# Optimization experiments

Hardware: AMD Instinct MI355X
Metric: run time of the kernel (lower is better)

Reference implementation:

```python
import jax, jax.numpy as jnp
import numpy as np

N, E, IN, HID, OUT = 50000, 800000, 128, 128, 4
EPS = 1e-16  # PyG softmax denominator epsilon


def setup_inputs() -> dict:
    key = jax.random.key(0)
    ks = jax.random.split(key, 12)
    g = lambda k, shp, fan: jax.random.normal(k, shp, jnp.float32) * (1.0 / np.sqrt(fan))
    return {
        "x": jax.random.normal(ks[0], (N, IN), jnp.float32),
        "edge_index": jax.random.randint(ks[1], (2, E), 0, N),
        "W1": g(ks[2], (IN, HID), IN),
        "att_l1": g(ks[3], (HID,), HID),
        "att_r1": g(ks[4], (HID,), HID),
        "b1": jnp.zeros((HID,), jnp.float32),
        "W2": g(ks[5], (HID, HID), HID),
        "att_l2": g(ks[6], (HID,), HID),
        "att_r2": g(ks[7], (HID,), HID),
        "b2": jnp.zeros((HID,), jnp.float32),
        "Wc": g(ks[8], (2 * HID, OUT), 2 * HID),
        "bc": jnp.zeros((OUT,), jnp.float32),
    }


def supergat_layer(x, src, dst, W, att_l, att_r, b, n_nodes):
    """SuperGATConv, attention_type='MX', heads=1, concat, eval mode (no dropout)."""
    h = x @ W                                   # [N, C] linear transform (no bias)
    hj, hi = h[src], h[dst]                     # gather source / target feats per edge [E', C]
    logits = jnp.sum(hi * hj, axis=-1)          # MX dot-product logits [E']
    alpha = hj @ att_l + hi @ att_r             # GAT-style additive score [E']
    alpha = alpha * jax.nn.sigmoid(logits)      # MX gating
    # segment softmax over destination node
    amax = jax.ops.segment_max(alpha, dst, num_segments=n_nodes)
    ea = jnp.exp(alpha - amax[dst])
    denom = jax.ops.segment_sum(ea, dst, num_segments=n_nodes)
    w = ea / (denom[dst] + EPS)
    # scatter-aggregate weighted messages
    out = jax.ops.segment_sum(hj * w[:, None], dst, num_segments=n_nodes)
    return out + b


def reference(x, edge_index, W1, att_l1, att_r1, b1, W2, att_l2, att_r2, b2, Wc, bc):
    row, col = edge_index[0], edge_index[1]
    loop = jnp.arange(N)
    src = jnp.concatenate([row, loop])          # add self-loops (PyG default)
    dst = jnp.concatenate([col, loop])
    h = supergat_layer(x, src, dst, W1, att_l1, att_r1, b1, N)
    h = jax.nn.relu(h)
    h = supergat_layer(h, src, dst, W2, att_l2, att_r2, b2, N)
    edge_emb = jnp.concatenate([h[row], h[col]], axis=-1)  # [E, 2*HID]
    return edge_emb @ Wc + bc                    # [E, OUT]
```

## Files before the change

### kernel.cpp

```cpp
#include <hip/hip_runtime.h>
#include <hip/hip_fp16.h>
#include <math.h>

#define C 128
#define EPSV 1e-16f
#define BCAP 64

typedef _Float16 half2v __attribute__((ext_vector_type(2)));
typedef _Float16 half8v __attribute__((ext_vector_type(8)));
typedef float float4v __attribute__((ext_vector_type(4)));

__device__ __forceinline__ float fdot2(half2v a, half2v b, float c) {
#if __has_builtin(__builtin_amdgcn_fdot2)
    return __builtin_amdgcn_fdot2(a, b, c, false);
#else
    return c + (float)a.x * (float)b.x + (float)a.y * (float)b.y;
#endif
}

__device__ __forceinline__ void unpack8(uint4 a, uint4 b, half2v* h) {
    h[0] = __builtin_bit_cast(half2v, a.x);
    h[1] = __builtin_bit_cast(half2v, a.y);
    h[2] = __builtin_bit_cast(half2v, a.z);
    h[3] = __builtin_bit_cast(half2v, a.w);
    h[4] = __builtin_bit_cast(half2v, b.x);
    h[5] = __builtin_bit_cast(half2v, b.y);
    h[6] = __builtin_bit_cast(half2v, b.z);
    h[7] = __builtin_bit_cast(half2v, b.w);
}


__global__ __launch_bounds__(256) void zero_kernel(int* __restrict__ p, int n) {
    int i = blockIdx.x * 256 + threadIdx.x;
    if (i < n) p[i] = 0;
}

__global__ __launch_bounds__(256) void fill_kernel(const int* __restrict__ rowA, const int* __restrict__ colA,
                                                   int* __restrict__ cursor, int* __restrict__ bucket, int e) {
    int i = blockIdx.x * 256 + threadIdx.x;
    if (i < e) {
        int c = colA[i];
        int p = atomicAdd(&cursor[c], 1);
        if (p < BCAP) bucket[c * BCAP + p] = rowA[i];
    }
}


template <bool SRC16>
__global__ __launch_bounds__(256) void gemm_att_mfma(const void* __restrict__ Asrc, const float* __restrict__ W,
                                                     const float* __restrict__ attl, const float* __restrict__ attr,
                                                     __half* __restrict__ Hh, float* __restrict__ al,
                                                     float* __restrict__ ar, int M) {
    __shared__ __half Ah[64][136];
    __shared__ __half Wt[128][136];

    int t = threadIdx.x;
    int lane = t & 63;
    int w = t >> 6;
    int quad = lane >> 4;
    int n16 = lane & 15;
    int row0 = blockIdx.x * 64;

    {
        int k = t >> 1;
        int cbase = (t & 1) * 64;
        const float4* Wr = (const float4*)(W + (size_t)k * C + cbase);
        #pragma unroll
        for (int q = 0; q < 16; q++) {
            float4 wv = Wr[q];
            int c = cbase + q * 4;
            Wt[c][k]     = __float2half(wv.x);
            Wt[c + 1][k] = __float2half(wv.y);
            Wt[c + 2][k] = __float2half(wv.z);
            Wt[c + 3][k] = __float2half(wv.w);
        }
    }
    {
        int r = t >> 2;
        int ks = (t & 3) * 32;
        int gr = row0 + r;
        if (SRC16) {
            const uint4* src = (const uint4*)((const __half*)Asrc + (size_t)gr * C + ks);
            uint4 z = make_uint4(0, 0, 0, 0);
            #pragma unroll
            for (int q = 0; q < 4; q++) {
                uint4 v = (gr < M) ? src[q] : z;
                *(uint4*)&Ah[r][ks + q * 8] = v;
            }
        } else {
            const float4* src = (const float4*)((const float*)Asrc + (size_t)gr * C + ks);
            #pragma unroll
            for (int q = 0; q < 8; q++) {
                float4 v = (gr < M) ? src[q] : make_float4(0.f, 0.f, 0.f, 0.f);
                __half2 lo = __floats2half2_rn(v.x, v.y);
                __half2 hi2 = __floats2half2_rn(v.z, v.w);
                uint2 pk;
                pk.x = *(unsigned int*)&lo;
                pk.y = *(unsigned int*)&hi2;
                *(uint2*)&Ah[r][ks + q * 4] = pk;
            }
        }
    }
    __syncthreads();

    float4v acc[8];
    #pragma unroll
    for (int ct = 0; ct < 8; ct++) acc[ct] = (float4v){0.f, 0.f, 0.f, 0.f};
    int mrow = w * 16 + n16;
    #pragma unroll
    for (int ks = 0; ks < 4; ks++) {
        int k0 = ks * 32 + quad * 8;
        half8v a = *(half8v*)&Ah[mrow][k0];
        #pragma unroll
        for (int ct = 0; ct < 8; ct++) {
            half8v b = *(half8v*)&Wt[ct * 16 + n16][k0];
            acc[ct] = __builtin_amdgcn_mfma_f32_16x16x32_f16(a, b, acc[ct], 0, 0, 0);
        }
    }

    #pragma unroll
    for (int ct = 0; ct < 8; ct++) {
        #pragma unroll
        for (int r = 0; r < 4; r++) {
            Ah[w * 16 + quad * 4 + r][ct * 16 + n16] = __float2half(acc[ct][r]);
        }
    }
    __syncthreads();

    {
        int r = t >> 2;
        int seg = (t & 3) * 32;
        int gr = row0 + r;
        uint4 d[4];
        #pragma unroll
        for (int q = 0; q < 4; q++) d[q] = *(uint4*)&Ah[r][seg + q * 8];
        float pl = 0.f, pr = 0.f;
        #pragma unroll
        for (int q = 0; q < 4; q++) {
            half2v hv[4];
            hv[0] = __builtin_bit_cast(half2v, d[q].x);
            hv[1] = __builtin_bit_cast(half2v, d[q].y);
            hv[2] = __builtin_bit_cast(half2v, d[q].z);
            hv[3] = __builtin_bit_cast(half2v, d[q].w);
            #pragma unroll
            for (int j = 0; j < 4; j++) {
                float2 f = make_float2((float)hv[j].x, (float)hv[j].y);
                int c = seg + q * 8 + j * 2;
                pl += f.x * attl[c] + f.y * attl[c + 1];
                pr += f.x * attr[c] + f.y * attr[c + 1];
            }
        }
        if (gr < M) {
            uint4* dst = (uint4*)&Hh[(size_t)gr * C + seg];
            #pragma unroll
            for (int q = 0; q < 4; q++) dst[q] = d[q];
        }
        pl += __shfl_xor(pl, 1);
        pl += __shfl_xor(pl, 2);
        pr += __shfl_xor(pr, 1);
        pr += __shfl_xor(pr, 2);
        if ((t & 3) == 0 && gr < M) { al[gr] = pl; ar[gr] = pr; }
    }
}


__device__ __forceinline__ void agg_core8(const __half* __restrict__ Hh, const int* __restrict__ bucket,
                                          const int* __restrict__ cnt, const float* __restrict__ al,
                                          const float* __restrict__ ar, const float* __restrict__ bvec,
                                          int node, int sub, int k, float* out) {
    const uint4* hp = (const uint4*)&Hh[(size_t)node * C + 16 * k];
    uint4 ha = hp[0], hb = hp[1];
    half2v hi[8];
    unpack8(ha, hb, hi);

    float aln = al[node];
    float arn = ar[node];

    float ds = 0.f;
    #pragma unroll
    for (int j = 0; j < 8; j++) ds = fdot2(hi[j], hi[j], ds);
    ds += __shfl_xor(ds, 1);
    ds += __shfl_xor(ds, 2);
    ds += __shfl_xor(ds, 4);
    float pself = __expf((aln + arn) / (1.0f + __expf(-ds)));

    bool s0 = (sub == 0);
    float denom = s0 ? pself : 0.0f;
    float acc[16];
    #pragma unroll
    for (int j = 0; j < 8; j++) {
        acc[2 * j]     = s0 ? pself * (float)hi[j].x : 0.0f;
        acc[2 * j + 1] = s0 ? pself * (float)hi[j].y : 0.0f;
    }

    int deg = cnt[node];
    if (deg > BCAP) deg = BCAP;
    int base = node * BCAP;

    int i = sub;
    uint4 raC, rbC;
    float alsC = 0.f;
    if (i < deg) {
        int s = bucket[base + i];
        const uint4* rp = (const uint4*)&Hh[(size_t)s * C + 16 * k];
        raC = rp[0];
        rbC = rp[1];
        alsC = al[s];
    }
    while (i < deg) {
        uint4 ra = raC, rb = rbC;
        float als = alsC;
        int inext = i + 8;
        if (inext < deg) {
            int s = bucket[base + inext];
            const uint4* rp = (const uint4*)&Hh[(size_t)s * C + 16 * k];
            raC = rp[0];
            rbC = rp[1];
            alsC = al[s];
        }
        half2v hj[8];
        unpack8(ra, rb, hj);
        float d = 0.f;
        #pragma unroll
        for (int j = 0; j < 8; j++) d = fdot2(hi[j], hj[j], d);
        d += __shfl_xor(d, 1);
        d += __shfl_xor(d, 2);
        d += __shfl_xor(d, 4);
        float p = __expf((als + arn) / (1.0f + __expf(-d)));
        denom += p;
        #pragma unroll
        for (int j = 0; j < 8; j++) {
            acc[2 * j]     += p * (float)hj[j].x;
            acc[2 * j + 1] += p * (float)hj[j].y;
        }
        i = inext;
    }

    denom += __shfl_xor(denom, 8);
    denom += __shfl_xor(denom, 16);
    denom += __shfl_xor(denom, 32);
    #pragma unroll
    for (int off = 8; off <= 32; off <<= 1) {
        #pragma unroll
        for (int j = 0; j < 16; j++) acc[j] += __shfl_xor(acc[j], off);
    }

    float inv = 1.0f / (denom + EPSV);
    const float4* bp = (const float4*)&bvec[16 * k];
    float4 b0 = bp[0], b1 = bp[1], b2 = bp[2], b3 = bp[3];
    out[0] = acc[0] * inv + b0.x;   out[1] = acc[1] * inv + b0.y;
    out[2] = acc[2] * inv + b0.z;   out[3] = acc[3] * inv + b0.w;
    out[4] = acc[4] * inv + b1.x;   out[5] = acc[5] * inv + b1.y;
    out[6] = acc[6] * inv + b1.z;   out[7] = acc[7] * inv + b1.w;
    out[8] = acc[8] * inv + b2.x;   out[9] = acc[9] * inv + b2.y;
    out[10] = acc[10] * inv + b2.z; out[11] = acc[11] * inv + b2.w;
    out[12] = acc[12] * inv + b3.x; out[13] = acc[13] * inv + b3.y;
    out[14] = acc[14] * inv + b3.z; out[15] = acc[15] * inv + b3.w;
}

__global__ __launch_bounds__(256) void agg_kernel(const __half* __restrict__ Hh, const int* __restrict__ bucket,
                                                  const int* __restrict__ cnt, const float* __restrict__ al,
                                                  const float* __restrict__ ar, const float* __restrict__ bvec,
                                                  __half* __restrict__ O, int n) {
    int node = blockIdx.x * 4 + (threadIdx.x >> 6);
    int lane = threadIdx.x & 63;
    if (node >= n) return;
    int sub = lane >> 3;
    int k = lane & 7;
    float out[16];
    agg_core8(Hh, bucket, cnt, al, ar, bvec, node, sub, k, out);
    if (sub == 0) {
        uint4 pk[2];
        #pragma unroll
        for (int h = 0; h < 2; h++) {
            unsigned int u[4];
            #pragma unroll
            for (int q = 0; q < 4; q++) {
                int j = h * 8 + q * 2;
                __half2 hv = __floats2half2_rn(fmaxf(out[j], 0.f), fmaxf(out[j + 1], 0.f));
                u[q] = *(unsigned int*)&hv;
            }
            pk[h] = make_uint4(u[0], u[1], u[2], u[3]);
        }
        uint4* dst = (uint4*)&O[(size_t)node * C + 16 * k];
        dst[0] = pk[0];
        dst[1] = pk[1];
    }
}

__global__ __launch_bounds__(256) void agg_proj_kernel(const __half* __restrict__ Hh, const int* __restrict__ bucket,
                                                       const int* __restrict__ cnt, const float* __restrict__ al,
                                                       const float* __restrict__ ar, const float* __restrict__ bvec,
                                                       const float* __restrict__ Wc, float* __restrict__ P1,
                                                       float* __restrict__ P2, int n) {
    int node = blockIdx.x * 4 + (threadIdx.x >> 6);
    int lane = threadIdx.x & 63;
    if (node >= n) return;
    int sub = lane >> 3;
    int k = lane & 7;
    float out[16];
    agg_core8(Hh, bucket, cnt, al, ar, bvec, node, sub, k, out);

    int o = sub & 3;
    const float* wcol = Wc + ((size_t)((sub >> 2) * C + 16 * k)) * 4 + o;
    float p = 0.f;
    #pragma unroll
    for (int j = 0; j < 16; j++) p += out[j] * wcol[j * 4];
    p += __shfl_xor(p, 1);
    p += __shfl_xor(p, 2);
    p += __shfl_xor(p, 4);
    if (k == 0) {
        if (sub < 4) P1[(size_t)node * 4 + o] = p;
        else         P2[(size_t)node * 4 + o] = p;
    }
}

__global__ __launch_bounds__(256) void edge_out_kernel(const float4* __restrict__ P1, const float4* __restrict__ P2,
                                                       const int* __restrict__ rowA, const int* __restrict__ colA,
                                                       const float* __restrict__ bc, float4* __restrict__ out, int e) {
    int i = blockIdx.x * 256 + threadIdx.x;
    if (i >= e) return;
    float4 a = P1[rowA[i]];
    float4 b = P2[colA[i]];
    float4 bcv = *(const float4*)bc;
    out[i] = make_float4(a.x + b.x + bcv.x, a.y + b.y + bcv.y, a.z + b.z + bcv.z, a.w + b.w + bcv.w);
}


extern "C" void kernel_launch(void* const* d_in, const int* in_sizes, int n_in,
                              void* d_out, int out_size, void* d_ws, size_t ws_size,
                              hipStream_t stream) {
    const float* x     = (const float*)d_in[0];
    const int*   ei    = (const int*)d_in[1];
    const float* W1    = (const float*)d_in[2];
    const float* attl1 = (const float*)d_in[3];
    const float* attr1 = (const float*)d_in[4];
    const float* b1    = (const float*)d_in[5];
    const float* W2    = (const float*)d_in[6];
    const float* attl2 = (const float*)d_in[7];
    const float* attr2 = (const float*)d_in[8];
    const float* b2    = (const float*)d_in[9];
    const float* Wc    = (const float*)d_in[10];
    const float* bc    = (const float*)d_in[11];
    float* out = (float*)d_out;

    const int N = in_sizes[0] / C;
    const int E = in_sizes[1] / 2;
    const int* rowA = ei;
    const int* colA = ei + E;

    __half* Hh     = (__half*)d_ws;
    __half* G2in   = Hh + (size_t)N * C;
    float*  al     = (float*)(G2in + (size_t)N * C);
    float*  ar     = al + N;
    int*    cursor = (int*)(ar + N);
    int*    bucket = cursor + N;
    float*  P1     = (float*)(bucket + (size_t)N * BCAP);
    float*  P2     = P1 + (size_t)N * 4;

    const int nbN = (N + 255) / 256;
    const int nbE = (E + 255) / 256;
    const int gemmBlocks = (N + 63) / 64;
    const int nodeBlocks = (N + 3) / 4;

    zero_kernel<<<nbN, 256, 0, stream>>>(cursor, N);
    fill_kernel<<<nbE, 256, 0, stream>>>(rowA, colA, cursor, bucket, E);

    gemm_att_mfma<false><<<gemmBlocks, 256, 0, stream>>>(x, W1, attl1, attr1, Hh, al, ar, N);
    agg_kernel<<<nodeBlocks, 256, 0, stream>>>(Hh, bucket, cursor, al, ar, b1, G2in, N);

    gemm_att_mfma<true><<<gemmBlocks, 256, 0, stream>>>(G2in, W2, attl2, attr2, Hh, al, ar, N);
    agg_proj_kernel<<<nodeBlocks, 256, 0, stream>>>(Hh, bucket, cursor, al, ar, b2, Wc, P1, P2, N);

    edge_out_kernel<<<nbE, 256, 0, stream>>>((const float4*)P1, (const float4*)P2, rowA, colA, bc, (float4*)out, E);
}
```

Baseline: 321.7 us.

## Pretranspose weights to fp16, convert x upfront, deepen gather prefetch in aggregation

Adds separate kernels that convert x to fp16 and transpose and convert W1/W2 into fp16 buffers once. Each GEMM block then reads A and W fragments straight from global memory instead of staging them in LDS, which removes the per-block W transpose and the first LDS sync. The aggregation loop now prefetches two neighbor rows ahead instead of one, to hide gather latency. The trade-offs are an extra full pass over x, two extra launches, and W fragments re-read from global/L2 by every block rather than from shared memory.

```diff
diff --git a/kernel.cpp b/kernel.cpp
--- a/kernel.cpp
+++ b/kernel.cpp
@@ -46,13 +46,40 @@
 }
 
 
-template <bool SRC16>
-__global__ __launch_bounds__(256) void gemm_att_mfma(const void* __restrict__ Asrc, const float* __restrict__ W,
+__global__ __launch_bounds__(256) void convert_x_kernel(const float* __restrict__ x, __half* __restrict__ x16, int n8) {
+    int i = blockIdx.x * 256 + threadIdx.x;
+    if (i >= n8) return;
+    float4 a = ((const float4*)x)[2 * i];
+    float4 b = ((const float4*)x)[2 * i + 1];
+    __half2 h0 = __floats2half2_rn(a.x, a.y);
+    __half2 h1 = __floats2half2_rn(a.z, a.w);
+    __half2 h2 = __floats2half2_rn(b.x, b.y);
+    __half2 h3 = __floats2half2_rn(b.z, b.w);
+    uint4 pk;
+    pk.x = *(unsigned int*)&h0;
+    pk.y = *(unsigned int*)&h1;
+    pk.z = *(unsigned int*)&h2;
+    pk.w = *(unsigned int*)&h3;
+    ((uint4*)x16)[i] = pk;
+}
+
+__global__ __launch_bounds__(256) void prep_w_kernel(const float* __restrict__ W1, const float* __restrict__ W2,
+                                                     __half* __restrict__ Wt1, __half* __restrict__ Wt2) {
+    int id = blockIdx.x * 256 + threadIdx.x;
+    const float* W = (id < 16384) ? W1 : W2;
+    __half* Wt = (id < 16384) ? Wt1 : Wt2;
+    int e = id & 16383;
+    int c = e >> 7;
+    int k = e & 127;
+    Wt[c * C + k] = __float2half(W[(size_t)k * C + c]);
+}
+
+
+__global__ __launch_bounds__(256) void gemm_att_mfma(const __half* __restrict__ A16, const __half* __restrict__ Wt,
                                                      const float* __restrict__ attl, const float* __restrict__ attr,
                                                      __half* __restrict__ Hh, float* __restrict__ al,
                                                      float* __restrict__ ar, int M) {
     __shared__ __half Ah[64][136];
-    __shared__ __half Wt[128][136];
 
     int t = threadIdx.x;
     int lane = t & 63;
@@ -61,59 +88,21 @@
     int n16 = lane & 15;
     int row0 = blockIdx.x * 64;
 
-    {
-        int k = t >> 1;
-        int cbase = (t & 1) * 64;
-        const float4* Wr = (const float4*)(W + (size_t)k * C + cbase);
-        #pragma unroll
-        for (int q = 0; q < 16; q++) {
-            float4 wv = Wr[q];
-            int c = cbase + q * 4;
-            Wt[c][k]     = __float2half(wv.x);
-            Wt[c + 1][k] = __float2half(wv.y);
-            Wt[c + 2][k] = __float2half(wv.z);
-            Wt[c + 3][k] = __float2half(wv.w);
-        }
-    }
-    {
-        int r = t >> 2;
-        int ks = (t & 3) * 32;
-        int gr = row0 + r;
-        if (SRC16) {
-            const uint4* src = (const uint4*)((const __half*)Asrc + (size_t)gr * C + ks);
-            uint4 z = make_uint4(0, 0, 0, 0);
-            #pragma unroll
-            for (int q = 0; q < 4; q++) {
-                uint4 v = (gr < M) ? src[q] : z;
-                *(uint4*)&Ah[r][ks + q * 8] = v;
-            }
-        } else {
-            const float4* src = (const float4*)((const float*)Asrc + (size_t)gr * C + ks);
-            #pragma unroll
-            for (int q = 0; q < 8; q++) {
-                float4 v = (gr < M) ? src[q] : make_float4(0.f, 0.f, 0.f, 0.f);
-                __half2 lo = __floats2half2_rn(v.x, v.y);
-                __half2 hi2 = __floats2half2_rn(v.z, v.w);
-                uint2 pk;
-                pk.x = *(unsigned int*)&lo;
-                pk.y = *(unsigned int*)&hi2;
-                *(uint2*)&Ah[r][ks + q * 4] = pk;
-            }
-        }
-    }
-    __syncthreads();
+    int mrow = row0 + w * 16 + n16;
+    bool mvalid = mrow < M;
+    const __half* arow = A16 + (size_t)mrow * C;
 
     float4v acc[8];
     #pragma unroll
     for (int ct = 0; ct < 8; ct++) acc[ct] = (float4v){0.f, 0.f, 0.f, 0.f};
-    int mrow = w * 16 + n16;
+
     #pragma unroll
     for (int ks = 0; ks < 4; ks++) {
         int k0 = ks * 32 + quad * 8;
-        half8v a = *(half8v*)&Ah[mrow][k0];
+        half8v a = mvalid ? *(const half8v*)&arow[k0] : (half8v)(_Float16)0;
         #pragma unroll
         for (int ct = 0; ct < 8; ct++) {
-            half8v b = *(half8v*)&Wt[ct * 16 + n16][k0];
+            half8v b = *(const half8v*)&Wt[(size_t)(ct * 16 + n16) * C + k0];
             acc[ct] = __builtin_amdgcn_mfma_f32_16x16x32_f16(a, b, acc[ct], 0, 0, 0);
         }
     }
@@ -168,14 +157,30 @@
                                           const int* __restrict__ cnt, const float* __restrict__ al,
                                           const float* __restrict__ ar, const float* __restrict__ bvec,
                                           int node, int sub, int k, float* out) {
+    int deg = cnt[node];
     const uint4* hp = (const uint4*)&Hh[(size_t)node * C + 16 * k];
     uint4 ha = hp[0], hb = hp[1];
+    float aln = al[node];
+    float arn = ar[node];
+    if (deg > BCAP) deg = BCAP;
+    int base = node * BCAP;
+
+    int i = sub;
+    uint4 ra0 = {}, rb0 = {}, ra1 = {}, rb1 = {};
+    float al0 = 0.f, al1 = 0.f;
+    if (i < deg) {
+        int s = bucket[base + i];
+        const uint4* rp = (const uint4*)&Hh[(size_t)s * C + 16 * k];
+        ra0 = rp[0]; rb0 = rp[1]; al0 = al[s];
+    }
+    if (i + 8 < deg) {
+        int s = bucket[base + i + 8];
+        const uint4* rp = (const uint4*)&Hh[(size_t)s * C + 16 * k];
+        ra1 = rp[0]; rb1 = rp[1]; al1 = al[s];
+    }
+
     half2v hi[8];
     unpack8(ha, hb, hi);
-
-    float aln = al[node];
-    float arn = ar[node];
-
     float ds = 0.f;
     #pragma unroll
     for (int j = 0; j < 8; j++) ds = fdot2(hi[j], hi[j], ds);
@@ -193,47 +198,32 @@
         acc[2 * j + 1] = s0 ? pself * (float)hi[j].y : 0.0f;
     }
 
-    int deg = cnt[node];
-    if (deg > BCAP) deg = BCAP;
-    int base = node * BCAP;
-
-    int i = sub;
-    uint4 raC, rbC;
-    float alsC = 0.f;
-    if (i < deg) {
-        int s = bucket[base + i];
-        const uint4* rp = (const uint4*)&Hh[(size_t)s * C + 16 * k];
-        raC = rp[0];
-        rbC = rp[1];
-        alsC = al[s];
-    }
     while (i < deg) {
-        uint4 ra = raC, rb = rbC;
-        float als = alsC;
-        int inext = i + 8;
-        if (inext < deg) {
-            int s = bucket[base + inext];
+        uint4 ca = ra0, cb = rb0;
+        float cal = al0;
+        ra0 = ra1; rb0 = rb1; al0 = al1;
+        int ipf = i + 16;
+        if (ipf < deg) {
+            int s = bucket[base + ipf];
             const uint4* rp = (const uint4*)&Hh[(size_t)s * C + 16 * k];
-            raC = rp[0];
-            rbC = rp[1];
-            alsC = al[s];
+            ra1 = rp[0]; rb1 = rp[1]; al1 = al[s];
         }
         half2v hj[8];
-        unpack8(ra, rb, hj);
+        unpack8(ca, cb, hj);
         float d = 0.f;
         #pragma unroll
         for (int j = 0; j < 8; j++) d = fdot2(hi[j], hj[j], d);
         d += __shfl_xor(d, 1);
         d += __shfl_xor(d, 2);
         d += __shfl_xor(d, 4);
-        float p = __expf((als + arn) / (1.0f + __expf(-d)));
+        float p = __expf((cal + arn) / (1.0f + __expf(-d)));
         denom += p;
         #pragma unroll
         for (int j = 0; j < 8; j++) {
             acc[2 * j]     += p * (float)hj[j].x;
             acc[2 * j + 1] += p * (float)hj[j].y;
         }
-        i = inext;
+        i += 8;
     }
 
     denom += __shfl_xor(denom, 8);
@@ -351,7 +341,10 @@
 
     __half* Hh     = (__half*)d_ws;
     __half* G2in   = Hh + (size_t)N * C;
-    float*  al     = (float*)(G2in + (size_t)N * C);
+    __half* X16    = G2in + (size_t)N * C;
+    __half* Wt1    = X16 + (size_t)N * C;
+    __half* Wt2    = Wt1 + C * C;
+    float*  al     = (float*)(Wt2 + C * C);
     float*  ar     = al + N;
     int*    cursor = (int*)(ar + N);
     int*    bucket = cursor + N;
@@ -362,14 +355,17 @@
     const int nbE = (E + 255) / 256;
     const int gemmBlocks = (N + 63) / 64;
     const int nodeBlocks = (N + 3) / 4;
+    const int n8 = N * C / 8;
 
     zero_kernel<<<nbN, 256, 0, stream>>>(cursor, N);
     fill_kernel<<<nbE, 256, 0, stream>>>(rowA, colA, cursor, bucket, E);
-
-    gemm_att_mfma<false><<<gemmBlocks, 256, 0, stream>>>(x, W1, attl1, attr1, Hh, al, ar, N);
+    convert_x_kernel<<<(n8 + 255) / 256, 256, 0, stream>>>(x, X16, n8);
+    prep_w_kernel<<<128, 256, 0, stream>>>(W1, W2, Wt1, Wt2);
+
+    gemm_att_mfma<<<gemmBlocks, 256, 0, stream>>>(X16, Wt1, attl1, attr1, Hh, al, ar, N);
     agg_kernel<<<nodeBlocks, 256, 0, stream>>>(Hh, bucket, cursor, al, ar, b1, G2in, N);
 
-    gemm_att_mfma<true><<<gemmBlocks, 256, 0, stream>>>(G2in, W2, attl2, attr2, Hh, al, ar, N);
+    gemm_att_mfma<<<gemmBlocks, 256, 0, stream>>>(G2in, Wt2, attl2, attr2, Hh, al, ar, N);
     agg_proj_kernel<<<nodeBlocks, 256, 0, stream>>>(Hh, bucket, cursor, al, ar, b2, Wc, P1, P2, N);
 
     edge_out_kernel<<<nbE, 256, 0, stream>>>((const float4*)P1, (const float4*)P2, rowA, colA, bc, (float4*)out, E);
```

After: 346.4 us. 7.7% more time.
